# Performance work log

Measured on AMD Instinct MI355X. Metric: run time of the kernel, lower is better.

The kernel has to match this reference:

```python
import jax, jax.numpy as jnp
import numpy as np

B, T, D, H = 2, 2048, 1024, 16
HD = D // H  # 64


def setup_inputs() -> dict:
    key = jax.random.key(0)
    ks = jax.random.split(key, 9)
    w = lambda k, shp: (jax.random.normal(k, shp, jnp.float32) * 0.02)
    return {
        "x": jax.random.normal(ks[0], (B, T, D), jnp.float32),
        "Wq": w(ks[1], (D, D)), "bq": jnp.zeros((D,), jnp.float32),
        "Wk": w(ks[2], (D, D)), "bk": jnp.zeros((D,), jnp.float32),
        "Wv": w(ks[3], (D, D)), "bv": jnp.zeros((D,), jnp.float32),
        "Wo": w(ks[4], (D, D)), "bo": jnp.zeros((D,), jnp.float32),
        "Wqs": w(ks[5], (3, HD)), "bqs": jnp.zeros((3,), jnp.float32),
        "Wks": w(ks[6], (3, HD)), "bks": jnp.zeros((3,), jnp.float32),
        "Wvs": w(ks[7], (3, HD)), "bvs": jnp.zeros((3,), jnp.float32),
        "temp": jnp.float32(1.0),
    }


def reference(x, Wq, bq, Wk, bk, Wv, bv, Wo, bo, Wqs, bqs, Wks, bks, Wvs, bvs, temp):
    Bx, Tx, Dx = x.shape
    # project and split heads: [B,H,T,HD]
    split = lambda y: y.reshape(Bx, Tx, H, HD).transpose(0, 2, 1, 3)
    q = split(x @ Wq.T + bq)
    k = split(x @ Wk.T + bk)
    v = split(x @ Wv.T + bv)
    # STP projections to 3-d: [B,H,T,3]
    q_stp = q @ Wqs.T + bqs
    k3 = k @ Wks.T + bks
    v3 = v @ Wvs.T + bvs
    # cross-product term (note: original's layernormed k_sub/v_sub are dead code)
    cross_kv = jnp.cross(k3, v3, axis=-1)  # [B,H,T,3]
    scores = (jnp.einsum('bhqd,bhkd->bhqk', q, k)
              + jnp.einsum('bhqc,bhkc->bhqk', q_stp, cross_kv)) * temp
    attn = jax.nn.softmax(scores, axis=-1)
    out = jnp.einsum('bhqk,bhkd->bhqd', attn, v)  # [B,H,T,HD]
    out = out.transpose(0, 2, 1, 3).reshape(Bx, Tx, Dx)
    return out @ Wo.T + bo
```

## Files before the change

kernel.cpp:

```cpp
#include <hip/hip_runtime.h>
#include <stdint.h>

typedef unsigned short u16;
typedef unsigned int u32;
typedef __attribute__((ext_vector_type(8))) short bf16x8;
typedef __attribute__((ext_vector_type(4))) float f32x4;

__device__ __forceinline__ u16 f2b(float f) {
    union { float f; u32 u; } t; t.f = f;
    return (u16)((t.u + 0x7FFFu + ((t.u >> 16) & 1u)) >> 16);
}
__device__ __forceinline__ u32 pack2(float a, float b) {
    return (u32)f2b(a) | ((u32)f2b(b) << 16);
}

__device__ __forceinline__ void async_cp16(const u16* g, const u16* lds_base) {
    __builtin_amdgcn_global_load_lds(
        (const __attribute__((address_space(1))) void*)(uintptr_t)g,
        (__attribute__((address_space(3))) void*)(u32)(uintptr_t)lds_base,
        16, 0, 0);
}

__global__ void cast_all_kernel(const float* __restrict__ x,
                                const float* __restrict__ Wq, const float* __restrict__ Wk,
                                const float* __restrict__ Wv, const float* __restrict__ Wo,
                                u16* __restrict__ xb, u16* __restrict__ Wqb, u16* __restrict__ Wkb,
                                u16* __restrict__ Wvb, u16* __restrict__ Wob) {
    int i = blockIdx.x * blockDim.x + threadIdx.x;
    const float* s; u16* d; int off;
    if (i < 1048576) { s = x; d = xb; off = i; }
    else {
        int j = i - 1048576;
        int w = j >> 18; off = j & 262143;
        if (w == 0) { s = Wq; d = Wqb; }
        else if (w == 1) { s = Wk; d = Wkb; }
        else if (w == 2) { s = Wv; d = Wvb; }
        else { s = Wo; d = Wob; }
    }
    float4 f = ((const float4*)s)[off];
    ((uint2*)d)[off] = make_uint2(pack2(f.x, f.y), pack2(f.z, f.w));
}

__global__ __launch_bounds__(256) void gemm_qkv_kernel(
    const u16* __restrict__ xb,
    const u16* __restrict__ Wq, const u16* __restrict__ Wk, const u16* __restrict__ Wv,
    const float* __restrict__ bq, const float* __restrict__ bk, const float* __restrict__ bv,
    const float* __restrict__ Wqs, const float* __restrict__ bqs,
    const float* __restrict__ Wks, const float* __restrict__ bks,
    const float* __restrict__ Wvs, const float* __restrict__ bvs,
    const float* __restrict__ temp_p,
    u16* __restrict__ qe, u16* __restrict__ ke, u16* __restrict__ vT,
    float4* __restrict__ k3b, float4* __restrict__ v3b)
{
    __shared__ __align__(16) u16 As[2 * 64 * 32];
    __shared__ __align__(16) u16 Bs[2 * 128 * 32];
    const int tid = threadIdx.x;
    const int lane = tid & 63, w = tid >> 6;
    const int wm = w >> 1, wn = w & 1;
    const int l15 = lane & 15, quad = lane >> 4;
    const int M0 = blockIdx.y * 64, N0 = blockIdx.x * 128;
    const int bz = blockIdx.z;

    const u16* W = (bz == 0) ? Wq : (bz == 1) ? Wk : Wv;
    const float* bias = (bz == 0) ? bq : (bz == 1) ? bk : bv;
    const float* Wst = (bz == 0) ? Wqs : (bz == 1) ? Wks : Wvs;
    const float* bst = (bz == 0) ? bqs : (bz == 1) ? bks : bvs;

    f32x4 acc[2][4];
#pragma unroll
    for (int i = 0; i < 2; i++)
#pragma unroll
        for (int j = 0; j < 4; j++) acc[i][j] = (f32x4){0.f, 0.f, 0.f, 0.f};

    int ra = tid >> 2, ca = ((tid & 3) ^ (ra & 3)) * 8;
    const u16* Aga = xb + (size_t)(M0 + ra) * 1024 + ca;
    const u16* Bg0 = W + (size_t)(N0 + ra) * 1024 + ca;
    const u16* Bg1 = W + (size_t)(N0 + ra + 64) * 1024 + ca;
    const int aoff = (w * 64) * 8;
    const int boff0 = (w * 64) * 8;
    const int boff1 = (256 + w * 64) * 8;

    async_cp16(Aga, As + aoff);
    async_cp16(Bg0, Bs + boff0);
    async_cp16(Bg1, Bs + boff1);
    __syncthreads();

    for (int k0 = 0; k0 < 1024; k0 += 32) {
        const int buf = (k0 >> 5) & 1;
        const u16* Asr = As + buf * 2048;
        const u16* Bsr = Bs + buf * 4096;
        if (k0 + 32 < 1024) {
            const int nb_ = buf ^ 1;
            async_cp16(Aga + k0 + 32, As + nb_ * 2048 + aoff);
            async_cp16(Bg0 + k0 + 32, Bs + nb_ * 4096 + boff0);
            async_cp16(Bg1 + k0 + 32, Bs + nb_ * 4096 + boff1);
        }

        bf16x8 af[2], bf[4];
#pragma unroll
        for (int mi = 0; mi < 2; mi++)
            af[mi] = *(const bf16x8*)(Asr + (wm * 32 + mi * 16 + l15) * 32 + ((quad ^ (l15 & 3)) * 8));
#pragma unroll
        for (int ni = 0; ni < 4; ni++)
            bf[ni] = *(const bf16x8*)(Bsr + (wn * 64 + ni * 16 + l15) * 32 + ((quad ^ (l15 & 3)) * 8));
#pragma unroll
        for (int mi = 0; mi < 2; mi++)
#pragma unroll
            for (int ni = 0; ni < 4; ni++)
                acc[mi][ni] = __builtin_amdgcn_mfma_f32_16x16x32_bf16(af[mi], bf[ni], acc[mi][ni], 0, 0, 0);

        __syncthreads();
    }

    const float tau = temp_p[0] * 1.44269504088896f;
    const int nb = N0 + wn * 64;
    const int h = nb >> 6;
    float bias_v[4], wst_v[3][4];
#pragma unroll
    for (int ni = 0; ni < 4; ni++) {
        bias_v[ni] = bias[nb + ni * 16 + l15];
#pragma unroll
        for (int c = 0; c < 3; c++) wst_v[c][ni] = Wst[c * 64 + ni * 16 + l15];
    }
    const float bst0 = bst[0], bst1 = bst[1], bst2 = bst[2];

#pragma unroll
    for (int mi = 0; mi < 2; mi++) {
        int m0 = M0 + wm * 32 + mi * 16 + quad * 4;
        int b = m0 >> 11, t0 = m0 & 2047;
        float p0[4], p1[4], p2[4];
#pragma unroll
        for (int r = 0; r < 4; r++) {
            float a0 = 0.f, a1 = 0.f, a2 = 0.f;
#pragma unroll
            for (int ni = 0; ni < 4; ni++) {
                float v = acc[mi][ni][r] + bias_v[ni];
                a0 += v * wst_v[0][ni];
                a1 += v * wst_v[1][ni];
                a2 += v * wst_v[2][ni];
            }
#pragma unroll
            for (int off = 1; off < 16; off <<= 1) {
                a0 += __shfl_xor(a0, off);
                a1 += __shfl_xor(a1, off);
                a2 += __shfl_xor(a2, off);
            }
            p0[r] = a0 + bst0; p1[r] = a1 + bst1; p2[r] = a2 + bst2;
        }

        if (bz == 0) {
#pragma unroll
            for (int r = 0; r < 4; r++) {
                size_t row = (size_t)((b * 16 + h) * 2048 + (t0 + r));
                u16* qer = qe + row * 96;
#pragma unroll
                for (int ni = 0; ni < 4; ni++)
                    qer[ni * 16 + l15] = f2b((acc[mi][ni][r] + bias_v[ni]) * tau);
                if (l15 == 0) {
                    *(u32*)(qer + 64) = pack2(p0[r] * tau, p1[r] * tau);
                    *(u32*)(qer + 66) = (u32)f2b(p2[r] * tau);
                    uint2 z = make_uint2(0u, 0u);
#pragma unroll
                    for (int j = 68; j < 96; j += 4) *(uint2*)(qer + j) = z;
                }
            }
        } else if (bz == 1) {
#pragma unroll
            for (int r = 0; r < 4; r++) {
                size_t row = (size_t)((b * 16 + h) * 2048 + (t0 + r));
                u16* ker = ke + row * 96;
#pragma unroll
                for (int ni = 0; ni < 4; ni++)
                    ker[ni * 16 + l15] = f2b(acc[mi][ni][r] + bias_v[ni]);
                if (l15 == 0)
                    k3b[row] = make_float4(p0[r], p1[r], p2[r], 0.f);
            }
        } else {
#pragma unroll
            for (int ni = 0; ni < 4; ni++) {
                int hd = ni * 16 + l15;
                float v0 = acc[mi][ni][0] + bias_v[ni];
                float v1 = acc[mi][ni][1] + bias_v[ni];
                float v2 = acc[mi][ni][2] + bias_v[ni];
                float v3 = acc[mi][ni][3] + bias_v[ni];
                *(uint2*)(vT + ((size_t)((b * 16 + h) * 64 + hd)) * 2048 + t0) =
                    make_uint2(pack2(v0, v1), pack2(v2, v3));
            }
            if (l15 == 0) {
#pragma unroll
                for (int r = 0; r < 4; r++) {
                    size_t row = (size_t)((b * 16 + h) * 2048 + (t0 + r));
                    v3b[row] = make_float4(p0[r], p1[r], p2[r], 0.f);
                }
            }
        }
    }
}

__global__ void finish_ext_kernel(const float4* __restrict__ k3b, const float4* __restrict__ v3b,
                                  u16* __restrict__ ke)
{
    int row = blockIdx.x * blockDim.x + threadIdx.x;
    if (row >= 2 * 16 * 2048) return;
    float4 k3 = k3b[row];
    float4 v3 = v3b[row];
    float c0 = k3.y * v3.z - k3.z * v3.y;
    float c1 = k3.z * v3.x - k3.x * v3.z;
    float c2 = k3.x * v3.y - k3.y * v3.x;
    u16* ker = ke + (size_t)row * 96;
    *(u32*)(ker + 64) = pack2(c0, c1);
    *(u32*)(ker + 66) = (u32)f2b(c2);
    uint2 z = make_uint2(0u, 0u);
#pragma unroll
    for (int j = 68; j < 96; j += 4) *(uint2*)(ker + j) = z;
}

__global__ __launch_bounds__(256) void gemm_out_kernel(
    const u16* __restrict__ ao, const u16* __restrict__ Wo, const float* __restrict__ bo,
    float* __restrict__ out)
{
    __shared__ __align__(16) u16 As[2 * 64 * 32];
    __shared__ __align__(16) u16 Bs[2 * 128 * 32];
    const int tid = threadIdx.x;
    const int lane = tid & 63, w = tid >> 6;
    const int wm = w >> 1, wn = w & 1;
    const int l15 = lane & 15, quad = lane >> 4;
    const int M0 = blockIdx.y * 64, N0 = blockIdx.x * 128;

    f32x4 acc[2][4];
#pragma unroll
    for (int i = 0; i < 2; i++)
#pragma unroll
        for (int j = 0; j < 4; j++) acc[i][j] = (f32x4){0.f, 0.f, 0.f, 0.f};

    int ra = tid >> 2, ca = ((tid & 3) ^ (ra & 3)) * 8;
    const u16* Aga = ao + (size_t)(M0 + ra) * 1024 + ca;
    const u16* Bg0 = Wo + (size_t)(N0 + ra) * 1024 + ca;
    const u16* Bg1 = Wo + (size_t)(N0 + ra + 64) * 1024 + ca;
    const int aoff = (w * 64) * 8;
    const int boff0 = (w * 64) * 8;
    const int boff1 = (256 + w * 64) * 8;

    async_cp16(Aga, As + aoff);
    async_cp16(Bg0, Bs + boff0);
    async_cp16(Bg1, Bs + boff1);
    __syncthreads();

    for (int k0 = 0; k0 < 1024; k0 += 32) {
        const int buf = (k0 >> 5) & 1;
        const u16* Asr = As + buf * 2048;
        const u16* Bsr = Bs + buf * 4096;
        if (k0 + 32 < 1024) {
            const int nb_ = buf ^ 1;
            async_cp16(Aga + k0 + 32, As + nb_ * 2048 + aoff);
            async_cp16(Bg0 + k0 + 32, Bs + nb_ * 4096 + boff0);
            async_cp16(Bg1 + k0 + 32, Bs + nb_ * 4096 + boff1);
        }

        bf16x8 af[2], bf[4];
#pragma unroll
        for (int mi = 0; mi < 2; mi++)
            af[mi] = *(const bf16x8*)(Asr + (wm * 32 + mi * 16 + l15) * 32 + ((quad ^ (l15 & 3)) * 8));
#pragma unroll
        for (int ni = 0; ni < 4; ni++)
            bf[ni] = *(const bf16x8*)(Bsr + (wn * 64 + ni * 16 + l15) * 32 + ((quad ^ (l15 & 3)) * 8));
#pragma unroll
        for (int mi = 0; mi < 2; mi++)
#pragma unroll
            for (int ni = 0; ni < 4; ni++)
                acc[mi][ni] = __builtin_amdgcn_mfma_f32_16x16x32_bf16(af[mi], bf[ni], acc[mi][ni], 0, 0, 0);

        __syncthreads();
    }

#pragma unroll
    for (int mi = 0; mi < 2; mi++)
#pragma unroll
        for (int ni = 0; ni < 4; ni++) {
            int n = N0 + wn * 64 + ni * 16 + l15;
            float bias_n = bo[n];
            int m0 = M0 + wm * 32 + mi * 16 + quad * 4;
#pragma unroll
            for (int r = 0; r < 4; r++)
                out[(size_t)(m0 + r) * 1024 + n] = acc[mi][ni][r] + bias_n;
        }
}

__global__ __launch_bounds__(256, 2) void attn_kernel(
    const u16* __restrict__ qe, const u16* __restrict__ ke, const u16* __restrict__ vT,
    u16* __restrict__ out)
{
    __shared__ __align__(16) u16 smem[32768];
    u16* const KsA = smem;
    u16* const VtA = smem + 16384;
    u16* const PsB = smem + 24576;

    const int tid = threadIdx.x;
    const int lane = tid & 63, w = tid >> 6;
    const int kw = w & 1, qw = w >> 1;
    const int l15 = lane & 15, quad = lane >> 4;
    const int lsw = l15 & 7;
    const int bh = blockIdx.y;
    const int q0 = blockIdx.x * 128;

    const u16* qeb = qe + (size_t)bh * 2048 * 96;
    const u16* keb = ke + (size_t)bh * 2048 * 96;
    const u16* vTb = vT + (size_t)bh * 64 * 2048;

    bf16x8 bq[4][3];
#pragma unroll
    for (int s = 0; s < 4; s++) {
        const u16* qrow = qeb + (size_t)(q0 + qw * 64 + s * 16 + l15) * 96;
#pragma unroll
        for (int ks = 0; ks < 3; ks++) bq[s][ks] = *(const bf16x8*)(qrow + ks * 32 + quad * 8);
    }

    f32x4 O[4][4];
    float l_part[4];
#pragma unroll
    for (int s = 0; s < 4; s++) {
        l_part[s] = 0.f;
#pragma unroll
        for (int dt = 0; dt < 4; dt++) O[s][dt] = (f32x4){0.f, 0.f, 0.f, 0.f};
    }

    const int srow = tid >> 2, spart = tid & 3;
    const int sh = srow & 7;
    u16* Pw[4];
#pragma unroll
    for (int s = 0; s < 4; s++) Pw[s] = PsB + (size_t)(qw * 64 + s * 16 + l15) * 64;

    {
        const u16* kg = keb + (size_t)srow * 96;
        uint4 a0 = *(const uint4*)(kg + spart * 8);
        uint4 a1 = *(const uint4*)(kg + (spart + 4) * 8);
        uint4 a2 = *(const uint4*)(kg + (spart + 8) * 8);
        const u16* vg = vTb + (size_t)srow * 2048;
        uint4 b0 = *(const uint4*)(vg + spart * 8);
        uint4 b1 = *(const uint4*)(vg + (spart + 4) * 8);
        *(uint4*)(KsA + srow * 128 + ((spart    ) ^ sh) * 8) = a0;
        *(uint4*)(KsA + srow * 128 + ((spart + 4) ^ sh) * 8) = a1;
        *(uint4*)(KsA + srow * 128 + ((spart + 8) ^ sh) * 8) = a2;
        *(uint4*)(VtA + srow * 64 + ((spart    ) ^ sh) * 8) = b0;
        *(uint4*)(VtA + srow * 64 + ((spart + 4) ^ sh) * 8) = b1;
    }
    __syncthreads();

    uint4 kx0, kx1, kx2, vx0, vx1;
    for (int kb = 0; kb < 2048; kb += 64) {
        const int buf = (kb >> 6) & 1;
        const u16* Ks = KsA + buf * 8192;
        const u16* Vt = VtA + buf * 4096;
        u16* Ksn = KsA + (buf ^ 1) * 8192;
        u16* Vtn = VtA + (buf ^ 1) * 4096;
        const bool more = (kb + 64) < 2048;

        if (more) {
            const u16* kg = keb + (size_t)(kb + 64 + srow) * 96;
            kx0 = *(const uint4*)(kg + spart * 8);
            kx1 = *(const uint4*)(kg + (spart + 4) * 8);
            kx2 = *(const uint4*)(kg + (spart + 8) * 8);
            const u16* vg = vTb + (size_t)srow * 2048 + (kb + 64);
            vx0 = *(const uint4*)(vg + spart * 8);
            vx1 = *(const uint4*)(vg + (spart + 4) * 8);
        }

        f32x4 S[4][2];
#pragma unroll
        for (int s = 0; s < 4; s++)
#pragma unroll
            for (int nt = 0; nt < 2; nt++) S[s][nt] = (f32x4){0.f, 0.f, 0.f, 0.f};
#pragma unroll
        for (int ks = 0; ks < 3; ks++) {
            bf16x8 ak[2];
#pragma unroll
            for (int nt = 0; nt < 2; nt++)
                ak[nt] = *(const bf16x8*)(Ks + (kw * 32 + nt * 16 + l15) * 128 + (((ks * 4 + quad) ^ lsw) & 15) * 8);
#pragma unroll
            for (int s = 0; s < 4; s++)
#pragma unroll
                for (int nt = 0; nt < 2; nt++)
                    S[s][nt] = __builtin_amdgcn_mfma_f32_16x16x32_bf16(ak[nt], bq[s][ks], S[s][nt], 0, 0, 0);
        }

#pragma unroll
        for (int s = 0; s < 4; s++) {
            float sum = 0.f;
#pragma unroll
            for (int nt = 0; nt < 2; nt++)
#pragma unroll
                for (int r = 0; r < 4; r++) {
                    float p = __builtin_amdgcn_exp2f(S[s][nt][r]);
                    S[s][nt][r] = p;
                    sum += p;
                }
            l_part[s] += sum;
#pragma unroll
            for (int nt = 0; nt < 2; nt++) {
                int c = (kw * 4 + nt * 2 + (quad >> 1)) ^ lsw;
                *(uint2*)(Pw[s] + c * 8 + (quad & 1) * 4) =
                    make_uint2(pack2(S[s][nt][0], S[s][nt][1]), pack2(S[s][nt][2], S[s][nt][3]));
            }
        }

        {
            bf16x8 av[4];
#pragma unroll
            for (int dt = 0; dt < 4; dt++)
                av[dt] = *(const bf16x8*)(Vt + (dt * 16 + l15) * 64 + (((kw * 4 + quad) ^ lsw) & 7) * 8);
#pragma unroll
            for (int s = 0; s < 4; s++) {
                bf16x8 pb = *(const bf16x8*)(Pw[s] + (((kw * 4 + quad) ^ lsw) & 7) * 8);
#pragma unroll
                for (int dt = 0; dt < 4; dt++)
                    O[s][dt] = __builtin_amdgcn_mfma_f32_16x16x32_bf16(av[dt], pb, O[s][dt], 0, 0, 0);
            }
        }

        if (more) {
            *(uint4*)(Ksn + srow * 128 + ((spart    ) ^ sh) * 8) = kx0;
            *(uint4*)(Ksn + srow * 128 + ((spart + 4) ^ sh) * 8) = kx1;
            *(uint4*)(Ksn + srow * 128 + ((spart + 8) ^ sh) * 8) = kx2;
            *(uint4*)(Vtn + srow * 64 + ((spart    ) ^ sh) * 8) = vx0;
            *(uint4*)(Vtn + srow * 64 + ((spart + 4) ^ sh) * 8) = vx1;
        }
        __syncthreads();
    }

    float* const Ored = (float*)smem;
    float* const Lr = (float*)(smem + 20480);
    if (kw == 1) {
#pragma unroll
        for (int s = 0; s < 4; s++) {
            float l = l_part[s];
            l += __shfl_xor(l, 16);
            l += __shfl_xor(l, 32);
            if (lane < 16) Lr[qw * 64 + s * 16 + l15] = l;
            int qrow = qw * 64 + s * 16 + l15;
#pragma unroll
            for (int dt = 0; dt < 4; dt++) {
                int dc = dt ^ (l15 & 3);
                *(float4*)(Ored + qrow * 68 + dc * 16 + quad * 4) =
                    make_float4(O[s][dt][0], O[s][dt][1], O[s][dt][2], O[s][dt][3]);
            }
        }
    }
    __syncthreads();
    if (kw == 0) {
        const int b = bh >> 4, h = bh & 15;
#pragma unroll
        for (int s = 0; s < 4; s++) {
            float l = l_part[s];
            l += __shfl_xor(l, 16);
            l += __shfl_xor(l, 32);
            int qrow = qw * 64 + s * 16 + l15;
            l += Lr[qrow];
            float linv = 1.0f / l;
            int tq = q0 + qrow;
#pragma unroll
            for (int dt = 0; dt < 4; dt++) {
                int dc = dt ^ (l15 & 3);
                float4 o2 = *(const float4*)(Ored + qrow * 68 + dc * 16 + quad * 4);
                int d = h * 64 + dt * 16 + quad * 4;
                *(uint2*)(out + (size_t)(b * 2048 + tq) * 1024 + d) =
                    make_uint2(pack2((O[s][dt][0] + o2.x) * linv, (O[s][dt][1] + o2.y) * linv),
                               pack2((O[s][dt][2] + o2.z) * linv, (O[s][dt][3] + o2.w) * linv));
            }
        }
    }
}

extern "C" void kernel_launch(void* const* d_in, const int* in_sizes, int n_in,
                              void* d_out, int out_size, void* d_ws, size_t ws_size,
                              hipStream_t stream)
{
    (void)in_sizes; (void)n_in; (void)out_size; (void)ws_size;
    const float* x   = (const float*)d_in[0];
    const float* Wq  = (const float*)d_in[1];
    const float* bq  = (const float*)d_in[2];
    const float* Wk  = (const float*)d_in[3];
    const float* bk  = (const float*)d_in[4];
    const float* Wv  = (const float*)d_in[5];
    const float* bv  = (const float*)d_in[6];
    const float* Wo  = (const float*)d_in[7];
    const float* bo  = (const float*)d_in[8];
    const float* Wqs = (const float*)d_in[9];
    const float* bqs = (const float*)d_in[10];
    const float* Wks = (const float*)d_in[11];
    const float* bks = (const float*)d_in[12];
    const float* Wvs = (const float*)d_in[13];
    const float* bvs = (const float*)d_in[14];
    const float* temp = (const float*)d_in[15];

    char* ws = (char*)d_ws;
    u16* xb  = (u16*)(ws);
    u16* Wqb = (u16*)(ws + 8388608);
    u16* Wkb = (u16*)(ws + 10485760);
    u16* Wvb = (u16*)(ws + 12582912);
    u16* Wob = (u16*)(ws + 14680064);
    u16* qeb = (u16*)(ws + 16777216);
    u16* keb = (u16*)(ws + 29360128);
    u16* vTb = (u16*)(ws + 41943040);
    float4* k3b = (float4*)(ws + 50331648);
    float4* v3b = (float4*)(ws + 51380224);
    u16* aob = (u16*)(ws + 52428800);

    cast_all_kernel<<<8192, 256, 0, stream>>>(x, Wq, Wk, Wv, Wo, xb, Wqb, Wkb, Wvb, Wob);
    gemm_qkv_kernel<<<dim3(8, 64, 3), 256, 0, stream>>>(
        xb, Wqb, Wkb, Wvb, bq, bk, bv, Wqs, bqs, Wks, bks, Wvs, bvs, temp,
        qeb, keb, vTb, k3b, v3b);
    finish_ext_kernel<<<256, 256, 0, stream>>>(k3b, v3b, keb);
    attn_kernel<<<dim3(16, 32), 256, 0, stream>>>(qeb, keb, vTb, aob);
    gemm_out_kernel<<<dim3(8, 64), 256, 0, stream>>>(aob, Wob, bo, (float*)d_out);
}
```

Before: 230.7 us.

## Prefetch K/V tiles with async global-to-LDS loads, add MFMA priority and hw bf16 pack

```diff
diff --git a/kernel.cpp b/kernel.cpp
--- a/kernel.cpp
+++ b/kernel.cpp
@@ -12,6 +12,11 @@
 }
 __device__ __forceinline__ u32 pack2(float a, float b) {
     return (u32)f2b(a) | ((u32)f2b(b) << 16);
+}
+__device__ __forceinline__ u32 cvtpk2(float lo, float hi) {
+    u32 r;
+    asm("v_cvt_pk_bf16_f32 %0, %1, %2" : "=v"(r) : "v"(lo), "v"(hi));
+    return r;
 }
 
 __device__ __forceinline__ void async_cp16(const u16* g, const u16* lds_base) {
@@ -307,6 +312,24 @@
     const u16* keb = ke + (size_t)bh * 2048 * 96;
     const u16* vTb = vT + (size_t)bh * 64 * 2048;
 
+    size_t koff[4];
+#pragma unroll
+    for (int j = 0; j < 4; j++) {
+        int r = w * 16 + j * 4 + (lane >> 4);
+        koff[j] = (size_t)r * 96 + (size_t)((((lane & 15) ^ (r & 7)) * 8));
+    }
+    size_t voff[2];
+#pragma unroll
+    for (int j = 0; j < 2; j++) {
+        int r = w * 16 + j * 8 + (lane >> 3);
+        voff[j] = (size_t)r * 2048 + (size_t)((((lane & 7) ^ (r & 7)) * 8));
+    }
+
+#pragma unroll
+    for (int j = 0; j < 4; j++) async_cp16(keb + koff[j], KsA + w * 2048 + j * 512);
+#pragma unroll
+    for (int j = 0; j < 2; j++) async_cp16(vTb + voff[j], VtA + w * 1024 + j * 512);
+
     bf16x8 bq[4][3];
 #pragma unroll
     for (int s = 0; s < 4; s++) {
@@ -324,45 +347,25 @@
         for (int dt = 0; dt < 4; dt++) O[s][dt] = (f32x4){0.f, 0.f, 0.f, 0.f};
     }
 
-    const int srow = tid >> 2, spart = tid & 3;
-    const int sh = srow & 7;
     u16* Pw[4];
 #pragma unroll
     for (int s = 0; s < 4; s++) Pw[s] = PsB + (size_t)(qw * 64 + s * 16 + l15) * 64;
 
-    {
-        const u16* kg = keb + (size_t)srow * 96;
-        uint4 a0 = *(const uint4*)(kg + spart * 8);
-        uint4 a1 = *(const uint4*)(kg + (spart + 4) * 8);
-        uint4 a2 = *(const uint4*)(kg + (spart + 8) * 8);
-        const u16* vg = vTb + (size_t)srow * 2048;
-        uint4 b0 = *(const uint4*)(vg + spart * 8);
-        uint4 b1 = *(const uint4*)(vg + (spart + 4) * 8);
-        *(uint4*)(KsA + srow * 128 + ((spart    ) ^ sh) * 8) = a0;
-        *(uint4*)(KsA + srow * 128 + ((spart + 4) ^ sh) * 8) = a1;
-        *(uint4*)(KsA + srow * 128 + ((spart + 8) ^ sh) * 8) = a2;
-        *(uint4*)(VtA + srow * 64 + ((spart    ) ^ sh) * 8) = b0;
-        *(uint4*)(VtA + srow * 64 + ((spart + 4) ^ sh) * 8) = b1;
-    }
     __syncthreads();
 
-    uint4 kx0, kx1, kx2, vx0, vx1;
     for (int kb = 0; kb < 2048; kb += 64) {
         const int buf = (kb >> 6) & 1;
         const u16* Ks = KsA + buf * 8192;
         const u16* Vt = VtA + buf * 4096;
-        u16* Ksn = KsA + (buf ^ 1) * 8192;
-        u16* Vtn = VtA + (buf ^ 1) * 4096;
-        const bool more = (kb + 64) < 2048;
-
-        if (more) {
-            const u16* kg = keb + (size_t)(kb + 64 + srow) * 96;
-            kx0 = *(const uint4*)(kg + spart * 8);
-            kx1 = *(const uint4*)(kg + (spart + 4) * 8);
-            kx2 = *(const uint4*)(kg + (spart + 8) * 8);
-            const u16* vg = vTb + (size_t)srow * 2048 + (kb + 64);
-            vx0 = *(const uint4*)(vg + spart * 8);
-            vx1 = *(const uint4*)(vg + (spart + 4) * 8);
+
+        if (kb + 64 < 2048) {
+            u16* Ksn = KsA + (buf ^ 1) * 8192;
+            u16* Vtn = VtA + (buf ^ 1) * 4096;
+            const size_t kb96 = (size_t)(kb + 64) * 96;
+#pragma unroll
+            for (int j = 0; j < 4; j++) async_cp16(keb + kb96 + koff[j], Ksn + w * 2048 + j * 512);
+#pragma unroll
+            for (int j = 0; j < 2; j++) async_cp16(vTb + (size_t)(kb + 64) + voff[j], Vtn + w * 1024 + j * 512);
         }
 
         f32x4 S[4][2];
@@ -370,6 +373,8 @@
         for (int s = 0; s < 4; s++)
 #pragma unroll
             for (int nt = 0; nt < 2; nt++) S[s][nt] = (f32x4){0.f, 0.f, 0.f, 0.f};
+
+        __builtin_amdgcn_s_setprio(1);
 #pragma unroll
         for (int ks = 0; ks < 3; ks++) {
             bf16x8 ak[2];
@@ -382,6 +387,7 @@
                 for (int nt = 0; nt < 2; nt++)
                     S[s][nt] = __builtin_amdgcn_mfma_f32_16x16x32_bf16(ak[nt], bq[s][ks], S[s][nt], 0, 0, 0);
         }
+        __builtin_amdgcn_s_setprio(0);
 
 #pragma unroll
         for (int s = 0; s < 4; s++) {
@@ -399,7 +405,7 @@
             for (int nt = 0; nt < 2; nt++) {
                 int c = (kw * 4 + nt * 2 + (quad >> 1)) ^ lsw;
                 *(uint2*)(Pw[s] + c * 8 + (quad & 1) * 4) =
-                    make_uint2(pack2(S[s][nt][0], S[s][nt][1]), pack2(S[s][nt][2], S[s][nt][3]));
+                    make_uint2(cvtpk2(S[s][nt][0], S[s][nt][1]), cvtpk2(S[s][nt][2], S[s][nt][3]));
             }
         }
 
@@ -408,6 +414,7 @@
 #pragma unroll
             for (int dt = 0; dt < 4; dt++)
                 av[dt] = *(const bf16x8*)(Vt + (dt * 16 + l15) * 64 + (((kw * 4 + quad) ^ lsw) & 7) * 8);
+            __builtin_amdgcn_s_setprio(1);
 #pragma unroll
             for (int s = 0; s < 4; s++) {
                 bf16x8 pb = *(const bf16x8*)(Pw[s] + (((kw * 4 + quad) ^ lsw) & 7) * 8);
@@ -415,15 +422,9 @@
                 for (int dt = 0; dt < 4; dt++)
                     O[s][dt] = __builtin_amdgcn_mfma_f32_16x16x32_bf16(av[dt], pb, O[s][dt], 0, 0, 0);
             }
-        }
-
-        if (more) {
-            *(uint4*)(Ksn + srow * 128 + ((spart    ) ^ sh) * 8) = kx0;
-            *(uint4*)(Ksn + srow * 128 + ((spart + 4) ^ sh) * 8) = kx1;
-            *(uint4*)(Ksn + srow * 128 + ((spart + 8) ^ sh) * 8) = kx2;
-            *(uint4*)(Vtn + srow * 64 + ((spart    ) ^ sh) * 8) = vx0;
-            *(uint4*)(Vtn + srow * 64 + ((spart + 4) ^ sh) * 8) = vx1;
-        }
+            __builtin_amdgcn_s_setprio(0);
+        }
+
         __syncthreads();
     }
 
@@ -463,8 +464,8 @@
                 float4 o2 = *(const float4*)(Ored + qrow * 68 + dc * 16 + quad * 4);
                 int d = h * 64 + dt * 16 + quad * 4;
                 *(uint2*)(out + (size_t)(b * 2048 + tq) * 1024 + d) =
-                    make_uint2(pack2((O[s][dt][0] + o2.x) * linv, (O[s][dt][1] + o2.y) * linv),
-                               pack2((O[s][dt][2] + o2.z) * linv, (O[s][dt][3] + o2.w) * linv));
+                    make_uint2(cvtpk2((O[s][dt][0] + o2.x) * linv, (O[s][dt][1] + o2.y) * linv),
+                               cvtpk2((O[s][dt][2] + o2.z) * linv, (O[s][dt][3] + o2.w) * linv));
             }
         }
     }
```

New measurement: 224.5 us. -2.7%, faster.
